# Optimization experiments

Measured on AMD Instinct MI355X. Metric: run time of the kernel, lower is better.

Reference implementation:

```python
import jax, jax.numpy as jnp
import numpy as np

D = 256; NH = 8; NL = 4; NP = 4; HD = D // NH
SHAPES = np.array([[64, 64], [32, 32], [16, 16], [8, 8]], dtype=np.int32)  # (H, W) per level
LSI = np.array([0, 4096, 5120, 5376], dtype=np.int32)
B = 4; LQ = int(SHAPES.prod(axis=1).sum())  # 5440


def setup_inputs() -> dict:
    key = jax.random.key(0)
    ks = jax.random.split(key, 16)
    p = lambda i, shape, s=0.02: jax.random.normal(ks[i], shape, dtype=jnp.float32) * s
    return dict(
        src=jax.random.normal(ks[0], (B, LQ, D), dtype=jnp.float32),
        pos=jax.random.normal(ks[1], (B, LQ, D), dtype=jnp.float32),
        reference_points=jax.random.uniform(ks[2], (B, LQ, NL, 2), dtype=jnp.float32),
        spatial_shapes=jnp.asarray(SHAPES),
        level_start_index=jnp.asarray(LSI),
        Wv=p(3, (D, D)), bv=jnp.zeros((D,), jnp.float32),
        Woff=p(4, (D, NH * NL * NP * 2)), boff=p(5, (NH * NL * NP * 2,)),
        Wattn=p(6, (D, NH * NL * NP)), battn=p(7, (NH * NL * NP,)),
        Wout=p(8, (D, D)), bout=jnp.zeros((D,), jnp.float32),
        g1=jnp.ones((D,), jnp.float32), b1=jnp.zeros((D,), jnp.float32),
        W1=p(9, (D, D)), bb1=jnp.zeros((D,), jnp.float32),
        W2=p(10, (D, D)), bb2=jnp.zeros((D,), jnp.float32),
        g3=jnp.ones((D,), jnp.float32), b3=jnp.zeros((D,), jnp.float32),
    )


def _ln(x, g, b, eps=1e-5):
    m = jnp.mean(x, -1, keepdims=True)
    v = jnp.mean(jnp.square(x - m), -1, keepdims=True)
    return (x - m) * jax.lax.rsqrt(v + eps) * g + b


def _bilinear(vflat, Hl, Wl, loc):
    # vflat: [B, Hl*Wl, nh, hd]; loc: [B, Lq, nh, np, 2] normalized to [0,1]
    # align_corners=False, zero padding (matches F.grid_sample in MSDeformAttn)
    x = loc[..., 0] * Wl - 0.5
    y = loc[..., 1] * Hl - 0.5
    x0 = jnp.floor(x); y0 = jnp.floor(y)
    fx = x - x0; fy = y - y0
    x0 = x0.astype(jnp.int32); y0 = y0.astype(jnp.int32)
    Bb, Lq, nh, npnt = x0.shape
    hd = vflat.shape[-1]
    out = jnp.zeros((Bb, Lq, nh, npnt, hd), vflat.dtype)
    for dy in (0, 1):
        for dx in (0, 1):
            xi = x0 + dx; yi = y0 + dy
            w = (fx if dx else 1.0 - fx) * (fy if dy else 1.0 - fy)
            valid = (xi >= 0) & (xi < Wl) & (yi >= 0) & (yi < Hl)
            idx = jnp.clip(yi, 0, Hl - 1) * Wl + jnp.clip(xi, 0, Wl - 1)  # [B,Lq,nh,np]
            idx = idx.transpose(0, 1, 3, 2).reshape(Bb, Lq * npnt, nh, 1)
            g = jnp.take_along_axis(vflat, idx, axis=1)
            g = g.reshape(Bb, Lq, npnt, nh, hd).transpose(0, 1, 3, 2, 4)
            out = out + g * (w * valid.astype(w.dtype))[..., None]
    return out  # [B, Lq, nh, np, hd]


def _forward(src, pos, reference_points, spatial_shapes, level_start_index,
             Wv, bv, Woff, boff, Wattn, battn, Wout, bout,
             g1, b1, W1, bb1, W2, bb2, g3, b3):
    shapes = np.asarray(spatial_shapes)
    lsi = np.asarray(level_start_index)
    Bq, Lq, Dm = src.shape
    q = src + pos  # with_pos_embed
    value = (src @ Wv + bv).reshape(Bq, Lq, NH, HD)
    off = (q @ Woff + boff).reshape(Bq, Lq, NH, NL, NP, 2)
    aw = jax.nn.softmax((q @ Wattn + battn).reshape(Bq, Lq, NH, NL * NP), axis=-1)
    aw = aw.reshape(Bq, Lq, NH, NL, NP)
    # offset normalizer is (W, H) per level
    norm = jnp.stack([shapes[:, 1].astype(np.float32), shapes[:, 0].astype(np.float32)], axis=-1)
    loc = reference_points[:, :, None, :, None, :] + off / norm[None, None, None, :, None, :]
    attended = jnp.zeros((Bq, Lq, NH, HD), src.dtype)
    for l in range(shapes.shape[0]):
        Hl, Wl = int(shapes[l, 0]), int(shapes[l, 1])
        s = int(lsi[l])
        vflat = value[:, s:s + Hl * Wl]
        sampled = _bilinear(vflat, Hl, Wl, loc[:, :, :, l])  # [B,Lq,nh,np,hd]
        attended = attended + jnp.einsum('blhpd,blhp->blhd', sampled, aw[:, :, :, l])
    src2 = attended.reshape(Bq, Lq, Dm) @ Wout + bout
    # residual + LayerNorm (dropout is identity in eval)
    sxy = _ln(src + src2, g1, b1)
    # FFN (d_ffn == d_model here), residual + LayerNorm
    h = jax.nn.relu(sxy @ W1 + bb1)
    return _ln(sxy + (h @ W2 + bb2), g3, b3)


def reference(src, pos, reference_points, spatial_shapes, level_start_index,
              Wv, bv, Woff, boff, Wattn, battn, Wout, bout,
              g1, b1, W1, bb1, W2, bb2, g3, b3):
    return _forward(src, pos, reference_points, spatial_shapes, level_start_index,
                    Wv, bv, Woff, boff, Wattn, battn, Wout, bout,
                    g1, b1, W1, bb1, W2, bb2, g3, b3)
```

## Files before the change

### kernel.cpp

```cpp
#include <hip/hip_runtime.h>
#include <cstddef>
#include <cstdint>

#define M_TOK 21760
#define LQ_ 5440

typedef _Float16 f16x8 __attribute__((ext_vector_type(8)));
typedef _Float16 h2v __attribute__((ext_vector_type(2)));
typedef float f32x4v __attribute__((ext_vector_type(4)));
typedef _Float16 half4v __attribute__((ext_vector_type(4)));

__device__ __forceinline__ unsigned short f2h(float f) {
  return __builtin_bit_cast(unsigned short, (_Float16)f);
}

__global__ __launch_bounds__(256) void prep_k(
    const float* __restrict__ src, const float* __restrict__ pos,
    const float* __restrict__ Wv, const float* __restrict__ Woff,
    const float* __restrict__ Wattn, const float* __restrict__ Wout,
    const float* __restrict__ W1, const float* __restrict__ W2,
    unsigned short* __restrict__ s16, unsigned short* __restrict__ q16,
    unsigned short* __restrict__ G, char* __restrict__ wsbase)
{
  const int b = blockIdx.x;
  if (b < 5440) {
    const int i = b * 256 + threadIdx.x;
    const float4 s = ((const float4*)src)[i];
    const float4 p = ((const float4*)pos)[i];
    ushort4 a, q;
    a.x = f2h(s.x); a.y = f2h(s.y); a.z = f2h(s.z); a.w = f2h(s.w);
    q.x = f2h(s.x + p.x); q.y = f2h(s.y + p.y); q.z = f2h(s.z + p.z); q.w = f2h(s.w + p.w);
    ((ushort4*)s16)[i] = a;
    ((ushort4*)q16)[i] = q;
  } else if (b < 6848) {
    const int gid = (b - 5440) * 256 + threadIdx.x;
    const float* srcs[6] = {Wv, Woff, Wattn, Wout, W1, W2};
    const int starts[7] = {0, 65536, 131072, 163840, 229376, 294912, 360448};
    const int Nn[6] = {256, 256, 128, 256, 256, 256};
    int m = 0;
#pragma unroll
    for (int i = 1; i < 6; ++i) m += (gid >= starts[i]);
    const int local = gid - starts[m];
    const int n = local >> 8;
    const int k = local & 255;
    G[gid] = f2h(srcs[m][(size_t)k * Nn[m] + n]);
  } else {
    const int tid = threadIdx.x;
    const uint4 z = {0u, 0u, 0u, 0u};
    if (tid < 64) {
      ((uint4*)wsbase)[tid] = z;
    } else if (tid < 128) {
      ((uint4*)(wsbase + 1024 + (size_t)M_TOK * 512))[tid - 64] = z;
    }
  }
}

__global__ __launch_bounds__(256, 2) void gemm_qkv_k(
    const unsigned short* __restrict__ s16, const unsigned short* __restrict__ q16,
    const unsigned short* __restrict__ WvT, const unsigned short* __restrict__ WfT,
    const float* __restrict__ bv, const float* __restrict__ boff,
    const float* __restrict__ battn,
    unsigned short* __restrict__ value16, unsigned short* __restrict__ fused16)
{
  const int by = blockIdx.y;
  const bool isv = (by < 2);
  const unsigned short* A  = isv ? s16 : q16;
  const unsigned short* Wt = isv ? WvT : WfT;
  const int n0 = isv ? by * 128 : (by - 2) * 128;
  const int N  = isv ? 256 : 384;
  unsigned short* out16 = isv ? value16 : fused16;
  const float* bsel; int nsub;
  if (isv)            { bsel = bv;    nsub = 0; }
  else if (n0 < 256)  { bsel = boff;  nsub = 0; }
  else                { bsel = battn; nsub = 256; }

  __shared__ unsigned short As[128 * 64];
  __shared__ unsigned short Bs[128 * 64];
  const int t = threadIdx.x;
  const int lane = t & 63, wave = t >> 6;
  const int wm = wave >> 1, wn = wave & 1;
  const int m0 = blockIdx.x * 128;

  const int lrow = lane >> 3;
  const int pcol = (lane & 7) << 4;
  const int scol = pcol ^ (lrow << 4);

  f32x4v acc[4][4];
#pragma unroll
  for (int i = 0; i < 4; ++i)
#pragma unroll
    for (int j = 0; j < 4; ++j) acc[i][j] = (f32x4v){0.f, 0.f, 0.f, 0.f};

  const int fr = lane & 15;
  const int fkb = (lane >> 4) << 4;

  for (int k0 = 0; k0 < 256; k0 += 64) {
#pragma unroll
    for (int i = 0; i < 4; ++i) {
      const int row = wave * 32 + i * 8 + lrow;
      const unsigned short* g = A + (size_t)(m0 + row) * 256 + k0 + (scol >> 1);
      unsigned short* s = As + (wave * 32 + i * 8) * 64;
      __builtin_amdgcn_global_load_lds(
          (const __attribute__((address_space(1))) void*)g,
          (__attribute__((address_space(3))) void*)s, 16, 0, 0);
    }
#pragma unroll
    for (int i = 0; i < 4; ++i) {
      const int row = wave * 32 + i * 8 + lrow;
      const unsigned short* g = Wt + (size_t)(n0 + row) * 256 + k0 + (scol >> 1);
      unsigned short* s = Bs + (wave * 32 + i * 8) * 64;
      __builtin_amdgcn_global_load_lds(
          (const __attribute__((address_space(1))) void*)g,
          (__attribute__((address_space(3))) void*)s, 16, 0, 0);
    }
    __syncthreads();

    f16x8 af[4][2], bfr[4][2];
#pragma unroll
    for (int i = 0; i < 4; ++i) {
      const int row = wm * 64 + i * 16 + fr;
      const char* base = (const char*)As + row * 128;
#pragma unroll
      for (int kk = 0; kk < 2; ++kk)
        af[i][kk] = *(const f16x8*)(base + ((kk * 64 + fkb) ^ ((row & 7) << 4)));
    }
#pragma unroll
    for (int j = 0; j < 4; ++j) {
      const int row = wn * 64 + j * 16 + fr;
      const char* base = (const char*)Bs + row * 128;
#pragma unroll
      for (int kk = 0; kk < 2; ++kk)
        bfr[j][kk] = *(const f16x8*)(base + ((kk * 64 + fkb) ^ ((row & 7) << 4)));
    }
#pragma unroll
    for (int i = 0; i < 4; ++i)
#pragma unroll
      for (int j = 0; j < 4; ++j) {
        acc[i][j] = __builtin_amdgcn_mfma_f32_16x16x32_f16(af[i][0], bfr[j][0], acc[i][j], 0, 0, 0);
        acc[i][j] = __builtin_amdgcn_mfma_f32_16x16x32_f16(af[i][1], bfr[j][1], acc[i][j], 0, 0, 0);
      }
    __syncthreads();
  }

  const int fq = lane >> 4;
#pragma unroll
  for (int j = 0; j < 4; ++j) {
    const int n = n0 + wn * 64 + j * 16 + fr;
    const float bj = bsel[n - nsub];
#pragma unroll
    for (int i = 0; i < 4; ++i) {
#pragma unroll
      for (int r = 0; r < 4; ++r) {
        const int m = m0 + wm * 64 + i * 16 + fq * 4 + r;
        out16[(size_t)m * N + n] = f2h(acc[i][j][r] + bj);
      }
    }
  }
}

__global__ __launch_bounds__(256, 2) void gemm16_k(
    const unsigned short* __restrict__ A, const unsigned short* __restrict__ Wt,
    const float* __restrict__ bias, unsigned short* __restrict__ out16,
    int N, int relu)
{
  __shared__ unsigned short As[128 * 64];
  __shared__ unsigned short Bs[128 * 64];
  const int t = threadIdx.x;
  const int lane = t & 63, wave = t >> 6;
  const int wm = wave >> 1, wn = wave & 1;
  const int m0 = blockIdx.x * 128, n0 = blockIdx.y * 128;

  const int lrow = lane >> 3;
  const int pcol = (lane & 7) << 4;
  const int scol = pcol ^ (lrow << 4);

  f32x4v acc[4][4];
#pragma unroll
  for (int i = 0; i < 4; ++i)
#pragma unroll
    for (int j = 0; j < 4; ++j) acc[i][j] = (f32x4v){0.f, 0.f, 0.f, 0.f};

  const int fr = lane & 15;
  const int fkb = (lane >> 4) << 4;

  for (int k0 = 0; k0 < 256; k0 += 64) {
#pragma unroll
    for (int i = 0; i < 4; ++i) {
      const int row = wave * 32 + i * 8 + lrow;
      const unsigned short* g = A + (size_t)(m0 + row) * 256 + k0 + (scol >> 1);
      unsigned short* s = As + (wave * 32 + i * 8) * 64;
      __builtin_amdgcn_global_load_lds(
          (const __attribute__((address_space(1))) void*)g,
          (__attribute__((address_space(3))) void*)s, 16, 0, 0);
    }
#pragma unroll
    for (int i = 0; i < 4; ++i) {
      const int row = wave * 32 + i * 8 + lrow;
      const unsigned short* g = Wt + (size_t)(n0 + row) * 256 + k0 + (scol >> 1);
      unsigned short* s = Bs + (wave * 32 + i * 8) * 64;
      __builtin_amdgcn_global_load_lds(
          (const __attribute__((address_space(1))) void*)g,
          (__attribute__((address_space(3))) void*)s, 16, 0, 0);
    }
    __syncthreads();

    f16x8 af[4][2], bfr[4][2];
#pragma unroll
    for (int i = 0; i < 4; ++i) {
      const int row = wm * 64 + i * 16 + fr;
      const char* base = (const char*)As + row * 128;
#pragma unroll
      for (int kk = 0; kk < 2; ++kk)
        af[i][kk] = *(const f16x8*)(base + ((kk * 64 + fkb) ^ ((row & 7) << 4)));
    }
#pragma unroll
    for (int j = 0; j < 4; ++j) {
      const int row = wn * 64 + j * 16 + fr;
      const char* base = (const char*)Bs + row * 128;
#pragma unroll
      for (int kk = 0; kk < 2; ++kk)
        bfr[j][kk] = *(const f16x8*)(base + ((kk * 64 + fkb) ^ ((row & 7) << 4)));
    }
#pragma unroll
    for (int i = 0; i < 4; ++i)
#pragma unroll
      for (int j = 0; j < 4; ++j) {
        acc[i][j] = __builtin_amdgcn_mfma_f32_16x16x32_f16(af[i][0], bfr[j][0], acc[i][j], 0, 0, 0);
        acc[i][j] = __builtin_amdgcn_mfma_f32_16x16x32_f16(af[i][1], bfr[j][1], acc[i][j], 0, 0, 0);
      }
    __syncthreads();
  }

  const int fq = lane >> 4;
#pragma unroll
  for (int j = 0; j < 4; ++j) {
    const int n = n0 + wn * 64 + j * 16 + fr;
    const float bj = bias[n];
#pragma unroll
    for (int i = 0; i < 4; ++i) {
#pragma unroll
      for (int r = 0; r < 4; ++r) {
        const int m = m0 + wm * 64 + i * 16 + fq * 4 + r;
        float v = acc[i][j][r] + bj;
        if (relu) v = fmaxf(v, 0.f);
        out16[(size_t)m * N + n] = f2h(v);
      }
    }
  }
}

__global__ __launch_bounds__(512, 4) void gemm_ln_k(
    const unsigned short* __restrict__ A, const unsigned short* __restrict__ Wt,
    const float* __restrict__ bias, const float* __restrict__ res,
    const float* __restrict__ g, const float* __restrict__ b,
    float* __restrict__ outf, unsigned short* __restrict__ out16)
{
  __shared__ unsigned short As[32 * 64];
  __shared__ unsigned short Bs[256 * 64 + 288];
  const int t = threadIdx.x;
  const int lane = t & 63, wave = t >> 6;
  const int rt = wave & 1, cg = wave >> 1;
  const int m0 = blockIdx.x * 32;

  const int lrow = lane >> 3;
  const int pcol = (lane & 7) << 4;
  const int scol = pcol ^ (lrow << 4);

  f32x4v acc[4];
#pragma unroll
  for (int j = 0; j < 4; ++j) acc[j] = (f32x4v){0.f, 0.f, 0.f, 0.f};

  const int fr = lane & 15;
  const int fq = lane >> 4;
  const int fkb = fq << 4;

  for (int k0 = 0; k0 < 256; k0 += 64) {
    if (wave < 4) {
      const int row = wave * 8 + lrow;
      const unsigned short* gp = A + (size_t)(m0 + row) * 256 + k0 + (scol >> 1);
      unsigned short* s = As + (wave * 8) * 64;
      __builtin_amdgcn_global_load_lds(
          (const __attribute__((address_space(1))) void*)gp,
          (__attribute__((address_space(3))) void*)s, 16, 0, 0);
    }
#pragma unroll
    for (int i = 0; i < 4; ++i) {
      const int row = wave * 32 + i * 8 + lrow;
      const unsigned short* gp = Wt + (size_t)row * 256 + k0 + (scol >> 1);
      unsigned short* s = Bs + (wave * 32 + i * 8) * 64;
      __builtin_amdgcn_global_load_lds(
          (const __attribute__((address_space(1))) void*)gp,
          (__attribute__((address_space(3))) void*)s, 16, 0, 0);
    }
    __syncthreads();

    f16x8 af0, af1;
    {
      const int arow = rt * 16 + fr;
      const char* abase = (const char*)As + arow * 128;
      af0 = *(const f16x8*)(abase + ((0 + fkb) ^ ((arow & 7) << 4)));
      af1 = *(const f16x8*)(abase + ((64 + fkb) ^ ((arow & 7) << 4)));
    }
#pragma unroll
    for (int j = 0; j < 4; ++j) {
      const int brow = cg * 64 + j * 16 + fr;
      const char* bbase = (const char*)Bs + brow * 128;
      const f16x8 b0 = *(const f16x8*)(bbase + ((0 + fkb) ^ ((brow & 7) << 4)));
      const f16x8 b1 = *(const f16x8*)(bbase + ((64 + fkb) ^ ((brow & 7) << 4)));
      acc[j] = __builtin_amdgcn_mfma_f32_16x16x32_f16(af0, b0, acc[j], 0, 0, 0);
      acc[j] = __builtin_amdgcn_mfma_f32_16x16x32_f16(af1, b1, acc[j], 0, 0, 0);
    }
    __syncthreads();
  }

  float* Cs = (float*)Bs;
#pragma unroll
  for (int j = 0; j < 4; ++j) {
    const int col = cg * 64 + j * 16 + fr;
#pragma unroll
    for (int rr = 0; rr < 4; ++rr) {
      const int row = rt * 16 + fq * 4 + rr;
      Cs[row * 260 + col] = acc[j][rr];
    }
  }
  __syncthreads();

  const int lg = lane >> 4, li = lane & 15;
  const int row = wave * 4 + lg;
  const size_t rowoff = (size_t)(m0 + row) * 256;

  float4 v[4];
  float s = 0.f;
#pragma unroll
  for (int c4 = 0; c4 < 4; ++c4) {
    const int col = c4 * 64 + li * 4;
    float4 x = *(float4*)&Cs[row * 260 + col];
    const float4 bi = *(const float4*)&bias[col];
    const float4 rv = *(const float4*)&res[rowoff + col];
    x.x += bi.x + rv.x; x.y += bi.y + rv.y;
    x.z += bi.z + rv.z; x.w += bi.w + rv.w;
    v[c4] = x;
    s += x.x + x.y + x.z + x.w;
  }
#pragma unroll
  for (int o = 1; o < 16; o <<= 1) s += __shfl_xor(s, o);
  const float mean = s * (1.f / 256.f);
  float ss = 0.f;
#pragma unroll
  for (int c4 = 0; c4 < 4; ++c4) {
    const float d0 = v[c4].x - mean, d1 = v[c4].y - mean;
    const float d2 = v[c4].z - mean, d3 = v[c4].w - mean;
    ss += d0 * d0 + d1 * d1 + d2 * d2 + d3 * d3;
  }
#pragma unroll
  for (int o = 1; o < 16; o <<= 1) ss += __shfl_xor(ss, o);
  const float rstd = rsqrtf(ss * (1.f / 256.f) + 1e-5f);

#pragma unroll
  for (int c4 = 0; c4 < 4; ++c4) {
    const int col = c4 * 64 + li * 4;
    const float4 gv = *(const float4*)&g[col];
    const float4 bv = *(const float4*)&b[col];
    float4 o4;
    o4.x = (v[c4].x - mean) * rstd * gv.x + bv.x;
    o4.y = (v[c4].y - mean) * rstd * gv.y + bv.y;
    o4.z = (v[c4].z - mean) * rstd * gv.z + bv.z;
    o4.w = (v[c4].w - mean) * rstd * gv.w + bv.w;
    if (outf) *(float4*)(outf + rowoff + col) = o4;
    if (out16) {
      ushort4 o;
      o.x = f2h(o4.x); o.y = f2h(o4.y); o.z = f2h(o4.z); o.w = f2h(o4.w);
      *(ushort4*)(out16 + rowoff + col) = o;
    }
  }
}

__global__ __launch_bounds__(256, 6) void samp_k(
    const unsigned short* __restrict__ value16, const unsigned short* __restrict__ fused16,
    const float* __restrict__ ref, unsigned short* __restrict__ att16)
{
  const int b = blockIdx.x;
  const int wg = (b & 7) * 340 + (b >> 3);
  const int tok0 = wg * 8;

  __shared__ half4v swv[8][136];
  __shared__ int2   siv[8][136];
  const int t = threadIdx.x;
  const _Float16* fh = (const _Float16*)fused16;

#pragma unroll
  for (int it = 0; it < 4; ++it) {
    const int idx = it * 256 + t;
    const int ti = idx >> 7;
    const int e  = idx & 127;
    const int tok = tok0 + ti;
    const int h = e >> 4;
    const int lvl = (e >> 2) & 3;
    const int HW[4] = {64, 32, 16, 8};
    const int LS[4] = {0, 4096, 5120, 5376};
    const int Wl = HW[lvl];

    const float lg = (float)fh[(size_t)tok * 384 + 256 + e];
    float mx = lg;
#pragma unroll
    for (int o = 1; o < 16; o <<= 1) mx = fmaxf(mx, __shfl_xor(mx, o, 16));
    const float ex = __expf(lg - mx);
    float sm = ex;
#pragma unroll
    for (int o = 1; o < 16; o <<= 1) sm += __shfl_xor(sm, o, 16);
    const float a = ex / sm;

    const float ox = (float)fh[(size_t)tok * 384 + e * 2 + 0];
    const float oy = (float)fh[(size_t)tok * 384 + e * 2 + 1];
    const float rx = ref[(size_t)tok * 8 + lvl * 2 + 0];
    const float ry = ref[(size_t)tok * 8 + lvl * 2 + 1];
    const float x = rx * (float)Wl + ox - 0.5f;
    const float y = ry * (float)Wl + oy - 0.5f;
    const float x0f = floorf(x), y0f = floorf(y);
    const float fx = x - x0f, fy = y - y0f;
    const int x0 = (int)x0f, y0 = (int)y0f;

    const int xi1 = x0 + 1, yi1 = y0 + 1;
    const float wx0 = 1.f - fx, wx1 = fx, wy0 = 1.f - fy, wy1 = fy;
    const bool vx0 = (x0 >= 0) & (x0 < Wl), vx1 = (xi1 >= 0) & (xi1 < Wl);
    const bool vy0 = (y0 >= 0) & (y0 < Wl), vy1 = (yi1 >= 0) & (yi1 < Wl);
    half4v hw;
    hw.x = (_Float16)((vx0 & vy0) ? a * wx0 * wy0 : 0.f);
    hw.y = (_Float16)((vx1 & vy0) ? a * wx1 * wy0 : 0.f);
    hw.z = (_Float16)((vx0 & vy1) ? a * wx0 * wy1 : 0.f);
    hw.w = (_Float16)((vx1 & vy1) ? a * wx1 * wy1 : 0.f);
    const int ax  = min(max(x0, -1), Wl - 1);
    const int yc0 = min(max(y0, 0), Wl - 1);
    const int yc1 = min(max(yi1, 0), Wl - 1);
    int2 io;
    io.x = (LS[lvl] + yc0 * Wl + ax) << 9;
    io.y = (LS[lvl] + yc1 * Wl + ax) << 9;
    const int sl = e + h;
    swv[ti][sl] = hw;
    siv[ti][sl] = io;
  }
  __syncthreads();

  const int wave = t >> 6, lane = t & 63;
  const int ti = wave * 2 + (lane >> 5);
  const int h = (lane >> 2) & 7, dg = lane & 3;
  const int tok = tok0 + ti;
  const int vbase = (tok0 / LQ_) * LQ_;
  const char* vb = (const char*)(value16 + (size_t)vbase * 256);
  const int laneoff = h * 64 + dg * 16;
  h2v a0 = {0, 0}, a1 = {0, 0}, a2 = {0, 0}, a3 = {0, 0};
  const int ebase = h * 17;

#define CORNER(U, HW_, WI) {                                       \
    const h2v w2 = __builtin_shufflevector(HW_, HW_, WI, WI);      \
    a0 += w2 * __builtin_bit_cast(h2v, U.x);                       \
    a1 += w2 * __builtin_bit_cast(h2v, U.y);                       \
    a2 += w2 * __builtin_bit_cast(h2v, U.z);                       \
    a3 += w2 * __builtin_bit_cast(h2v, U.w); }

#pragma unroll
  for (int p = 0; p < 16; p += 2) {
    const half4v w0 = swv[ti][ebase + p];
    const half4v w1 = swv[ti][ebase + p + 1];
    const int2 i0 = siv[ti][ebase + p];
    const int2 i1 = siv[ti][ebase + p + 1];
    const char* p00 = vb + (i0.x + laneoff);
    const char* p01 = vb + (i0.y + laneoff);
    const char* p10 = vb + (i1.x + laneoff);
    const char* p11 = vb + (i1.y + laneoff);
    const uint4 u0 = *(const uint4*)(p00);
    const uint4 u1 = *(const uint4*)(p00 + 512);
    const uint4 u2 = *(const uint4*)(p01);
    const uint4 u3 = *(const uint4*)(p01 + 512);
    const uint4 u4 = *(const uint4*)(p10);
    const uint4 u5 = *(const uint4*)(p10 + 512);
    const uint4 u6 = *(const uint4*)(p11);
    const uint4 u7 = *(const uint4*)(p11 + 512);
    CORNER(u0, w0, 0) CORNER(u1, w0, 1) CORNER(u2, w0, 2) CORNER(u3, w0, 3)
    CORNER(u4, w1, 0) CORNER(u5, w1, 1) CORNER(u6, w1, 2) CORNER(u7, w1, 3)
  }
#undef CORNER

  uint4 o;
  o.x = __builtin_bit_cast(unsigned, a0);
  o.y = __builtin_bit_cast(unsigned, a1);
  o.z = __builtin_bit_cast(unsigned, a2);
  o.w = __builtin_bit_cast(unsigned, a3);
  *(uint4*)(att16 + (size_t)tok * 256 + h * 32 + dg * 8) = o;
}

extern "C" void kernel_launch(void* const* d_in, const int* in_sizes, int n_in,
                              void* d_out, int out_size, void* d_ws, size_t ws_size,
                              hipStream_t stream)
{
  const float* src   = (const float*)d_in[0];
  const float* pos   = (const float*)d_in[1];
  const float* ref   = (const float*)d_in[2];
  const float* Wv    = (const float*)d_in[5];
  const float* bv    = (const float*)d_in[6];
  const float* Woff  = (const float*)d_in[7];
  const float* boff  = (const float*)d_in[8];
  const float* Wattn = (const float*)d_in[9];
  const float* battn = (const float*)d_in[10];
  const float* Wout  = (const float*)d_in[11];
  const float* bout  = (const float*)d_in[12];
  const float* g1    = (const float*)d_in[13];
  const float* b1    = (const float*)d_in[14];
  const float* W1    = (const float*)d_in[15];
  const float* bb1   = (const float*)d_in[16];
  const float* W2    = (const float*)d_in[17];
  const float* bb2   = (const float*)d_in[18];
  const float* g3    = (const float*)d_in[19];
  const float* b3    = (const float*)d_in[20];

  float* out = (float*)d_out;
  char* ws = (char*)d_ws;
  const size_t M = M_TOK;

  float* bufA = (float*)ws;
  unsigned short* fused16 = (unsigned short*)(ws + M * 256 * 4);
  unsigned short* bufE = fused16 + M * 384;
  unsigned short* bufF = bufE + M * 256;
  unsigned short* bufG = bufF + M * 256;
  unsigned short* value16 = (unsigned short*)(ws + 1024);

  unsigned short* WvT     = bufG + 0;
  unsigned short* WfusedT = bufG + 65536;
  unsigned short* WoutT   = bufG + 163840;
  unsigned short* W1T     = bufG + 229376;
  unsigned short* W2T     = bufG + 294912;

  const dim3 blk(256);

  prep_k<<<dim3(6849), blk, 0, stream>>>(src, pos, Wv, Woff, Wattn, Wout, W1, W2,
                                         bufE, bufF, bufG, ws);
  gemm_qkv_k<<<dim3(170, 5), blk, 0, stream>>>(bufE, bufF, WvT, WfusedT,
                                               bv, boff, battn, value16, fused16);
  samp_k<<<dim3(2720), blk, 0, stream>>>(value16, fused16, ref, bufE);
  gemm_ln_k<<<dim3(680), dim3(512), 0, stream>>>(bufE, WoutT, bout, src, g1, b1, bufA, bufF);
  gemm16_k<<<dim3(170, 2), blk, 0, stream>>>(bufF, W1T, bb1, bufE, 256, 1);
  gemm_ln_k<<<dim3(680), dim3(512), 0, stream>>>(bufE, W2T, bb2, bufA, g3, b3, out, nullptr);
}
```

Before: 105.3 us.

## Store value in head-major layout and remap sampling lanes to pixel pairs

The value projection is now written head-major ([head][token][32]), so the two horizontally adjacent pixels for one head sit in a contiguous 128-byte span. The sampling kernel packs weights and row offsets into one 16-byte shared entry, has each lane load one 16-byte slice of two adjacent pixels, and merges the x0/x1 halves with a cross-lane shuffle. Each wave now handles two tokens per pass, aiming for more coalesced gathers and fewer shared-memory reads. The value GEMM epilogue gains scattered, strided 2-byte stores to build the new layout.

```diff
diff --git a/kernel.cpp b/kernel.cpp
--- a/kernel.cpp
+++ b/kernel.cpp
@@ -8,10 +8,13 @@
 typedef _Float16 f16x8 __attribute__((ext_vector_type(8)));
 typedef _Float16 h2v __attribute__((ext_vector_type(2)));
 typedef float f32x4v __attribute__((ext_vector_type(4)));
-typedef _Float16 half4v __attribute__((ext_vector_type(4)));
 
 __device__ __forceinline__ unsigned short f2h(float f) {
   return __builtin_bit_cast(unsigned short, (_Float16)f);
+}
+__device__ __forceinline__ unsigned packh2(float a, float b) {
+  h2v p; p[0] = (_Float16)a; p[1] = (_Float16)b;
+  return __builtin_bit_cast(unsigned, p);
 }
 
 __global__ __launch_bounds__(256) void prep_k(
@@ -60,15 +63,14 @@
     const unsigned short* __restrict__ WvT, const unsigned short* __restrict__ WfT,
     const float* __restrict__ bv, const float* __restrict__ boff,
     const float* __restrict__ battn,
-    unsigned short* __restrict__ value16, unsigned short* __restrict__ fused16)
+    unsigned short* __restrict__ value_hm, unsigned short* __restrict__ fused16)
 {
   const int by = blockIdx.y;
   const bool isv = (by < 2);
   const unsigned short* A  = isv ? s16 : q16;
   const unsigned short* Wt = isv ? WvT : WfT;
   const int n0 = isv ? by * 128 : (by - 2) * 128;
-  const int N  = isv ? 256 : 384;
-  unsigned short* out16 = isv ? value16 : fused16;
+  const int N  = 384;
   const float* bsel; int nsub;
   if (isv)            { bsel = bv;    nsub = 0; }
   else if (n0 < 256)  { bsel = boff;  nsub = 0; }
@@ -152,7 +154,12 @@
 #pragma unroll
       for (int r = 0; r < 4; ++r) {
         const int m = m0 + wm * 64 + i * 16 + fq * 4 + r;
-        out16[(size_t)m * N + n] = f2h(acc[i][j][r] + bj);
+        const unsigned short v = f2h(acc[i][j][r] + bj);
+        if (isv) {
+          value_hm[((size_t)(n >> 5) * M_TOK + m) * 32 + (n & 31)] = v;
+        } else {
+          fused16[(size_t)m * N + n] = v;
+        }
       }
     }
   }
@@ -376,17 +383,17 @@
 }
 
 __global__ __launch_bounds__(256, 6) void samp_k(
-    const unsigned short* __restrict__ value16, const unsigned short* __restrict__ fused16,
+    const unsigned short* __restrict__ value_hm, const unsigned short* __restrict__ fused16,
     const float* __restrict__ ref, unsigned short* __restrict__ att16)
 {
   const int b = blockIdx.x;
   const int wg = (b & 7) * 340 + (b >> 3);
   const int tok0 = wg * 8;
 
-  __shared__ half4v swv[8][136];
-  __shared__ int2   siv[8][136];
+  __shared__ uint4 sent[8][136];
   const int t = threadIdx.x;
   const _Float16* fh = (const _Float16*)fused16;
+  const int bb = (tok0 / LQ_) * LQ_;
 
 #pragma unroll
   for (int it = 0; it < 4; ++it) {
@@ -424,69 +431,93 @@
     const float wx0 = 1.f - fx, wx1 = fx, wy0 = 1.f - fy, wy1 = fy;
     const bool vx0 = (x0 >= 0) & (x0 < Wl), vx1 = (xi1 >= 0) & (xi1 < Wl);
     const bool vy0 = (y0 >= 0) & (y0 < Wl), vy1 = (yi1 >= 0) & (yi1 < Wl);
-    half4v hw;
-    hw.x = (_Float16)((vx0 & vy0) ? a * wx0 * wy0 : 0.f);
-    hw.y = (_Float16)((vx1 & vy0) ? a * wx1 * wy0 : 0.f);
-    hw.z = (_Float16)((vx0 & vy1) ? a * wx0 * wy1 : 0.f);
-    hw.w = (_Float16)((vx1 & vy1) ? a * wx1 * wy1 : 0.f);
+    const float w00 = (vx0 & vy0) ? a * wx0 * wy0 : 0.f;
+    const float w10 = (vx1 & vy0) ? a * wx1 * wy0 : 0.f;
+    const float w01 = (vx0 & vy1) ? a * wx0 * wy1 : 0.f;
+    const float w11 = (vx1 & vy1) ? a * wx1 * wy1 : 0.f;
     const int ax  = min(max(x0, -1), Wl - 1);
     const int yc0 = min(max(y0, 0), Wl - 1);
     const int yc1 = min(max(yi1, 0), Wl - 1);
-    int2 io;
-    io.x = (LS[lvl] + yc0 * Wl + ax) << 9;
-    io.y = (LS[lvl] + yc1 * Wl + ax) << 9;
-    const int sl = e + h;
-    swv[ti][sl] = hw;
-    siv[ti][sl] = io;
+    const int rowbase = h * M_TOK + bb + LS[lvl] + ax;
+    uint4 ent;
+    ent.x = packh2(w00, w10);
+    ent.y = packh2(w01, w11);
+    ent.z = (unsigned)((rowbase + yc0 * Wl) << 6);
+    ent.w = (unsigned)((rowbase + yc1 * Wl) << 6);
+    sent[ti][e + h] = ent;
   }
   __syncthreads();
 
   const int wave = t >> 6, lane = t & 63;
-  const int ti = wave * 2 + (lane >> 5);
-  const int h = (lane >> 2) & 7, dg = lane & 3;
-  const int tok = tok0 + ti;
-  const int vbase = (tok0 / LQ_) * LQ_;
-  const char* vb = (const char*)(value16 + (size_t)vbase * 256);
-  const int laneoff = h * 64 + dg * 16;
-  h2v a0 = {0, 0}, a1 = {0, 0}, a2 = {0, 0}, a3 = {0, 0};
+  const int h = lane >> 3, d8 = lane & 7;
+  const int xs = (d8 >> 2) & 1;
+  const int s4 = d8 & 3;
+  const int laneoff = d8 * 16;
   const int ebase = h * 17;
-
-#define CORNER(U, HW_, WI) {                                       \
-    const h2v w2 = __builtin_shufflevector(HW_, HW_, WI, WI);      \
-    a0 += w2 * __builtin_bit_cast(h2v, U.x);                       \
-    a1 += w2 * __builtin_bit_cast(h2v, U.y);                       \
-    a2 += w2 * __builtin_bit_cast(h2v, U.z);                       \
-    a3 += w2 * __builtin_bit_cast(h2v, U.w); }
-
-#pragma unroll
-  for (int p = 0; p < 16; p += 2) {
-    const half4v w0 = swv[ti][ebase + p];
-    const half4v w1 = swv[ti][ebase + p + 1];
-    const int2 i0 = siv[ti][ebase + p];
-    const int2 i1 = siv[ti][ebase + p + 1];
-    const char* p00 = vb + (i0.x + laneoff);
-    const char* p01 = vb + (i0.y + laneoff);
-    const char* p10 = vb + (i1.x + laneoff);
-    const char* p11 = vb + (i1.y + laneoff);
-    const uint4 u0 = *(const uint4*)(p00);
-    const uint4 u1 = *(const uint4*)(p00 + 512);
-    const uint4 u2 = *(const uint4*)(p01);
-    const uint4 u3 = *(const uint4*)(p01 + 512);
-    const uint4 u4 = *(const uint4*)(p10);
-    const uint4 u5 = *(const uint4*)(p10 + 512);
-    const uint4 u6 = *(const uint4*)(p11);
-    const uint4 u7 = *(const uint4*)(p11 + 512);
-    CORNER(u0, w0, 0) CORNER(u1, w0, 1) CORNER(u2, w0, 2) CORNER(u3, w0, 3)
-    CORNER(u4, w1, 0) CORNER(u5, w1, 1) CORNER(u6, w1, 2) CORNER(u7, w1, 3)
-  }
-#undef CORNER
-
-  uint4 o;
-  o.x = __builtin_bit_cast(unsigned, a0);
-  o.y = __builtin_bit_cast(unsigned, a1);
-  o.z = __builtin_bit_cast(unsigned, a2);
-  o.w = __builtin_bit_cast(unsigned, a3);
-  *(uint4*)(att16 + (size_t)tok * 256 + h * 32 + dg * 8) = o;
+  const int tiA = wave * 2, tiB = tiA + 1;
+  const char* vb = (const char*)value_hm;
+
+  h2v aA0 = {0,0}, aA1 = {0,0}, aA2 = {0,0}, aA3 = {0,0};
+  h2v aB0 = {0,0}, aB1 = {0,0}, aB2 = {0,0}, aB3 = {0,0};
+
+#define FMA4(A0,A1,A2,A3,U,W) {                                   \
+    A0 += W * __builtin_bit_cast(h2v, U.x);                       \
+    A1 += W * __builtin_bit_cast(h2v, U.y);                       \
+    A2 += W * __builtin_bit_cast(h2v, U.z);                       \
+    A3 += W * __builtin_bit_cast(h2v, U.w); }
+
+#pragma unroll
+  for (int pe = 0; pe < 16; pe += 2) {
+#pragma unroll
+    for (int q = 0; q < 2; ++q) {
+      const uint4 eA = sent[tiA][ebase + pe + q];
+      const uint4 eB = sent[tiB][ebase + pe + q];
+      const uint4 uA0 = *(const uint4*)(vb + ((int)eA.z + laneoff));
+      const uint4 uA1 = *(const uint4*)(vb + ((int)eA.w + laneoff));
+      const uint4 uB0 = *(const uint4*)(vb + ((int)eB.z + laneoff));
+      const uint4 uB1 = *(const uint4*)(vb + ((int)eB.w + laneoff));
+      const h2v wAy0 = __builtin_bit_cast(h2v, eA.x);
+      const h2v wAy1 = __builtin_bit_cast(h2v, eA.y);
+      const h2v wBy0 = __builtin_bit_cast(h2v, eB.x);
+      const h2v wBy1 = __builtin_bit_cast(h2v, eB.y);
+      const _Float16 wa0 = xs ? wAy0[1] : wAy0[0];
+      const _Float16 wa1 = xs ? wAy1[1] : wAy1[0];
+      const _Float16 wb0 = xs ? wBy0[1] : wBy0[0];
+      const _Float16 wb1 = xs ? wBy1[1] : wBy1[0];
+      h2v va0; va0[0] = wa0; va0[1] = wa0;
+      h2v va1; va1[0] = wa1; va1[1] = wa1;
+      h2v vb0; vb0[0] = wb0; vb0[1] = wb0;
+      h2v vb1; vb1[0] = wb1; vb1[1] = wb1;
+      FMA4(aA0, aA1, aA2, aA3, uA0, va0)
+      FMA4(aA0, aA1, aA2, aA3, uA1, va1)
+      FMA4(aB0, aB1, aB2, aB3, uB0, vb0)
+      FMA4(aB0, aB1, aB2, aB3, uB1, vb1)
+    }
+  }
+#undef FMA4
+
+#define COMB(A) {                                                  \
+    unsigned u = __builtin_bit_cast(unsigned, A);                  \
+    unsigned o = __shfl_xor((int)u, 4);                            \
+    A += __builtin_bit_cast(h2v, o); }
+  COMB(aA0) COMB(aA1) COMB(aA2) COMB(aA3)
+  COMB(aB0) COMB(aB1) COMB(aB2) COMB(aB3)
+#undef COMB
+
+  if (xs == 0) {
+    uint4 oA, oB;
+    oA.x = __builtin_bit_cast(unsigned, aA0);
+    oA.y = __builtin_bit_cast(unsigned, aA1);
+    oA.z = __builtin_bit_cast(unsigned, aA2);
+    oA.w = __builtin_bit_cast(unsigned, aA3);
+    oB.x = __builtin_bit_cast(unsigned, aB0);
+    oB.y = __builtin_bit_cast(unsigned, aB1);
+    oB.z = __builtin_bit_cast(unsigned, aB2);
+    oB.w = __builtin_bit_cast(unsigned, aB3);
+    const int tokA = tok0 + tiA, tokB = tok0 + tiB;
+    *(uint4*)(att16 + (size_t)tokA * 256 + h * 32 + s4 * 8) = oA;
+    *(uint4*)(att16 + (size_t)tokB * 256 + h * 32 + s4 * 8) = oB;
+  }
 }
 
 extern "C" void kernel_launch(void* const* d_in, const int* in_sizes, int n_in,
@@ -522,7 +553,7 @@
   unsigned short* bufE = fused16 + M * 384;
   unsigned short* bufF = bufE + M * 256;
   unsigned short* bufG = bufF + M * 256;
-  unsigned short* value16 = (unsigned short*)(ws + 1024);
+  unsigned short* value_hm = (unsigned short*)(ws + 1024);
 
   unsigned short* WvT     = bufG + 0;
   unsigned short* WfusedT = bufG + 65536;
@@ -535,8 +566,8 @@
   prep_k<<<dim3(6849), blk, 0, stream>>>(src, pos, Wv, Woff, Wattn, Wout, W1, W2,
                                          bufE, bufF, bufG, ws);
   gemm_qkv_k<<<dim3(170, 5), blk, 0, stream>>>(bufE, bufF, WvT, WfusedT,
-                                               bv, boff, battn, value16, fused16);
-  samp_k<<<dim3(2720), blk, 0, stream>>>(value16, fused16, ref, bufE);
+                                               bv, boff, battn, value_hm, fused16);
+  samp_k<<<dim3(2720), blk, 0, stream>>>(value_hm, fused16, ref, bufE);
   gemm_ln_k<<<dim3(680), dim3(512), 0, stream>>>(bufE, WoutT, bout, src, g1, b1, bufA, bufF);
   gemm16_k<<<dim3(170, 2), blk, 0, stream>>>(bufF, W1T, bb1, bufE, 256, 1);
   gemm_ln_k<<<dim3(680), dim3(512), 0, stream>>>(bufE, W2T, bb2, bufA, g3, b3, out, nullptr);
```

After: 109.3 us. 1.04x slower.
